# Kernel tuning notes

Hardware: AMD Instinct MI355X
Metric: run time of the kernel (lower is better)

Reference implementation:

```python
import jax, jax.numpy as jnp
import numpy as np

B, S, D, H, PF = 2, 2048, 1024, 16, 4096
HD = D // H
EPS = 1e-5


def _rope_tables(seq_len, dim, theta=10000.0):
    freqs = 1.0 / (theta ** (np.arange(0, dim, 2)[: dim // 2].astype(np.float32) / dim))
    ang = np.outer(np.arange(seq_len, dtype=np.float32), freqs)  # [S, D/2]
    return jnp.asarray(np.cos(ang)), jnp.asarray(np.sin(ang))


def setup_inputs() -> dict:
    key = jax.random.key(0)
    ks = jax.random.split(key, 16)
    s = 0.02
    inp = {
        "src": jax.random.normal(ks[0], (B, S, D), dtype=jnp.float32),
        "Wq": jax.random.normal(ks[1], (D, D), dtype=jnp.float32) * s,
        "bq": jnp.zeros((D,), jnp.float32),
        "Wk": jax.random.normal(ks[2], (D, D), dtype=jnp.float32) * s,
        "bk": jnp.zeros((D,), jnp.float32),
        "Wv": jax.random.normal(ks[3], (D, D), dtype=jnp.float32) * s,
        "bv": jnp.zeros((D,), jnp.float32),
        "Wo": jax.random.normal(ks[4], (D, D), dtype=jnp.float32) * s,
        "bo": jnp.zeros((D,), jnp.float32),
        "ln1_g": jnp.ones((D,), jnp.float32),
        "ln1_b": jnp.zeros((D,), jnp.float32),
        "W1": jax.random.normal(ks[5], (D, PF), dtype=jnp.float32) * s,
        "b1": jnp.zeros((PF,), jnp.float32),
        "W2": jax.random.normal(ks[6], (PF, D), dtype=jnp.float32) * s,
        "b2": jnp.zeros((D,), jnp.float32),
        "ln2_g": jnp.ones((D,), jnp.float32),
        "ln2_b": jnp.zeros((D,), jnp.float32),
    }
    cos, sin = _rope_tables(S, D)
    inp["rope_cos"] = cos
    inp["rope_sin"] = sin
    return inp


def _apply_rope(x, cos, sin):
    # x: [B, S, D]; rotate adjacent channel pairs as complex numbers (Meta LLaMA style)
    xp = x.reshape(x.shape[0], x.shape[1], -1, 2)
    a, b = xp[..., 0], xp[..., 1]
    c = cos[None, : x.shape[1]]
    s = sin[None, : x.shape[1]]
    out = jnp.stack([a * c - b * s, a * s + b * c], axis=-1)
    return out.reshape(x.shape)


def _layer_norm(x, g, b):
    mu = x.mean(-1, keepdims=True)
    var = ((x - mu) ** 2).mean(-1, keepdims=True)
    return (x - mu) * jax.lax.rsqrt(var + EPS) * g + b


def reference(src, Wq, bq, Wk, bk, Wv, bv, Wo, bo, ln1_g, ln1_b,
              W1, b1, W2, b2, ln2_g, ln2_b, rope_cos, rope_sin):
    bsz, seq, _ = src.shape
    Q = src @ Wq + bq
    K = src @ Wk + bk
    V = src @ Wv + bv
    Q = _apply_rope(Q, rope_cos, rope_sin)
    K = _apply_rope(K, rope_cos, rope_sin)
    # split heads: [B, H, S, HD]
    Q = Q.reshape(bsz, seq, H, HD).transpose(0, 2, 1, 3)
    K = K.reshape(bsz, seq, H, HD).transpose(0, 2, 1, 3)
    V = V.reshape(bsz, seq, H, HD).transpose(0, 2, 1, 3)
    scale = 1.0 / jnp.sqrt(jnp.float32(HD))
    energy = jnp.einsum("bhqd,bhkd->bhqk", Q, K) * scale
    attn = jax.nn.softmax(energy, axis=-1)
    x = jnp.einsum("bhqk,bhkd->bhqd", attn, V)
    x = x.transpose(0, 2, 1, 3).reshape(bsz, seq, D)
    attn_out = x @ Wo + bo
    # residual + LayerNorm
    h = _layer_norm(src + attn_out, ln1_g, ln1_b)
    # positionwise feedforward
    ff = jax.nn.relu(h @ W1 + b1) @ W2 + b2
    return _layer_norm(h + ff, ln2_g, ln2_b)
```

## Files before the change

kernel.cpp:

```cpp
#include <hip/hip_runtime.h>

#define SEQ 2048
#define DIM 1024
#define NH 16
#define HDIM 64
#define PFF 4096
#define NROWS 4096
#define BATCH 2
#define NQKV 3072

typedef unsigned short u16;
typedef unsigned int u32;
typedef __attribute__((ext_vector_type(8))) short short8;
typedef __attribute__((ext_vector_type(4))) float f32x4;
typedef __attribute__((ext_vector_type(16))) float f32x16;

__device__ inline float b2f(u16 u){ return __uint_as_float(((u32)u)<<16); }
__device__ inline u16 f2b(float f){
  u32 u = __float_as_uint(f);
  u32 r = u + 0x7FFFu + ((u>>16)&1u);
  return (u16)(r>>16);
}
__device__ __forceinline__ float fexp2(float x){
  float r; asm("v_exp_f32 %0, %1" : "=v"(r) : "v"(x)); return r;
}

#define AS1C(p) ((const __attribute__((address_space(1))) unsigned int*)(p))
#define AS3P(p) ((__attribute__((address_space(3))) unsigned int*)(p))

__global__ __launch_bounds__(256) void k_prep(
    const float* __restrict__ src, u16* __restrict__ Xbf,
    const float* __restrict__ Wq, const float* __restrict__ Wk,
    const float* __restrict__ Wv, const float* __restrict__ Wo,
    u16* __restrict__ WqkvT, u16* __restrict__ WoT,
    const float* __restrict__ W1, u16* __restrict__ W1T,
    const float* __restrict__ W2, u16* __restrict__ W2T,
    const float* __restrict__ bq, const float* __restrict__ bk,
    const float* __restrict__ bv, float* __restrict__ bqkv){
  __shared__ float tile[32][33];
  const int lid = blockIdx.x, tid = threadIdx.x;
  if (lid < 4096){
    int i = lid*256 + tid;
    float4 v = ((const float4*)src)[i];
    ushort4 o;
    o.x = f2b(v.x); o.y = f2b(v.y); o.z = f2b(v.z); o.w = f2b(v.w);
    ((ushort4*)Xbf)[i] = o;
    return;
  }
  int tx = tid & 31, ty = tid >> 5;
  if (lid < 8192){
    int rem = lid - 4096;
    int z = rem >> 10; rem &= 1023;
    const float* in = z==0 ? Wq : (z==1 ? Wk : (z==2 ? Wv : Wo));
    u16* out = (z<3) ? (WqkvT + (size_t)z*DIM*DIM) : WoT;
    int c0 = (rem & 31)*32, r0 = (rem >> 5)*32;
    #pragma unroll
    for (int i=0;i<4;++i)
      tile[ty+i*8][tx] = in[(size_t)(r0+ty+i*8)*DIM + c0 + tx];
    __syncthreads();
    #pragma unroll
    for (int i=0;i<4;++i)
      out[(size_t)(c0+ty+i*8)*DIM + r0 + tx] = f2b(tile[tx][ty+i*8]);
    return;
  }
  if (lid < 12288){
    int rem = lid - 8192;
    int c0 = (rem & 127)*32, r0 = (rem >> 7)*32;
    #pragma unroll
    for (int i=0;i<4;++i)
      tile[ty+i*8][tx] = W1[(size_t)(r0+ty+i*8)*PFF + c0 + tx];
    __syncthreads();
    #pragma unroll
    for (int i=0;i<4;++i)
      W1T[(size_t)(c0+ty+i*8)*DIM + r0 + tx] = f2b(tile[tx][ty+i*8]);
    return;
  }
  if (lid < 16384){
    int rem = lid - 12288;
    int c0 = (rem & 31)*32, r0 = (rem >> 5)*32;
    #pragma unroll
    for (int i=0;i<4;++i)
      tile[ty+i*8][tx] = W2[(size_t)(r0+ty+i*8)*DIM + c0 + tx];
    __syncthreads();
    #pragma unroll
    for (int i=0;i<4;++i)
      W2T[(size_t)(c0+ty+i*8)*PFF + r0 + tx] = f2b(tile[tx][ty+i*8]);
    return;
  }
  {
    int i = (lid - 16384)*256 + tid;
    if (i < NQKV)
      bqkv[i] = i < 1024 ? bq[i] : (i < 2048 ? bk[i-1024] : bv[i-2048]);
  }
}

template<bool RELU, bool BF16OUT, int SPLIT>
__global__ __launch_bounds__(512, 2) void k_gemm256(
    const u16* __restrict__ A, const u16* __restrict__ Bt,
    const float* __restrict__ bias, void* __restrict__ Cp,
    int M, int N, int Kc, int lda, int ldb){
  extern __shared__ char lds[];
  const int tid = threadIdx.x;
  const int lane = tid & 63, wid = tid >> 6;
  const int quad = lane >> 4, l15 = lane & 15;
  const int wm = wid >> 2, wn = wid & 3;
  const int ro = (l15*4 + quad)*16;
  const int srow = lane >> 2;
  const int sk   = (lane & 3)*8;
  const int nwg = gridDim.x * gridDim.y;
  int lid = blockIdx.y * gridDim.x + blockIdx.x;
  lid = (lid & 7) * (nwg >> 3) + (lid >> 3);
  const int bx = lid % gridDim.x, by = lid / gridDim.x;
  const int rowBase = by*256, colBase = bx*256;
  const u16* Az = A  + (size_t)blockIdx.z * Kc;
  const u16* Bz = Bt + (size_t)blockIdx.z * Kc;

  f32x4 acc[8][4] = {};

  auto stage2 = [&](int buf, int k0, int i){
    int idx = i*8 + wid;
    int rs = idx >> 1, ks = idx & 1;
    const u16* ga = Az + (size_t)(rowBase + rs*16 + srow)*lda + k0 + ks*32 + sk;
    __builtin_amdgcn_global_load_lds(AS1C(ga), AS3P(lds + buf*65536 + idx*1024), 16, 0, 0);
    const u16* gb = Bz + (size_t)(colBase + rs*16 + srow)*ldb + k0 + ks*32 + sk;
    __builtin_amdgcn_global_load_lds(AS1C(gb), AS3P(lds + buf*65536 + 32768 + idx*1024), 16, 0, 0);
  };

  #pragma unroll
  for (int i=0;i<4;++i) stage2(0, 0, i);
  __syncthreads();

  const int NT = Kc >> 6;
  #pragma unroll 1
  for (int t=0; t<NT; ++t){
    const int buf = t & 1;
    const bool pf = (t+1 < NT);
    const int k0n = (t+1)*64;
    char* Ab = lds + buf*65536;
    char* Bb = Ab + 32768;
    short8 a0[4][2], a1[4][2], b0[2][2], b1[2][2];

    #pragma unroll
    for (int mf=0; mf<4; ++mf)
      #pragma unroll
      for (int kk=0; kk<2; ++kk)
        a0[mf][kk] = *(const short8*)(Ab + ((wm*8+mf)*2+kk)*1024 + ro);
    #pragma unroll
    for (int nf=0; nf<2; ++nf)
      #pragma unroll
      for (int kk=0; kk<2; ++kk)
        b0[nf][kk] = *(const short8*)(Bb + ((wn*4+nf)*2+kk)*1024 + ro);
    if (pf){ stage2(buf^1, k0n, 0); stage2(buf^1, k0n, 1); }
    __builtin_amdgcn_s_barrier();
    __builtin_amdgcn_s_setprio(1);
    #pragma unroll
    for (int mf=0; mf<4; ++mf)
      #pragma unroll
      for (int nf=0; nf<2; ++nf)
        #pragma unroll
        for (int kk=0; kk<2; ++kk)
          acc[mf][nf] = __builtin_amdgcn_mfma_f32_16x16x32_bf16(a0[mf][kk], b0[nf][kk], acc[mf][nf], 0,0,0);
    __builtin_amdgcn_s_setprio(0);
    __builtin_amdgcn_s_barrier();

    #pragma unroll
    for (int nf=0; nf<2; ++nf)
      #pragma unroll
      for (int kk=0; kk<2; ++kk)
        b1[nf][kk] = *(const short8*)(Bb + ((wn*4+2+nf)*2+kk)*1024 + ro);
    if (pf){ stage2(buf^1, k0n, 2); stage2(buf^1, k0n, 3); }
    __builtin_amdgcn_s_barrier();
    __builtin_amdgcn_s_setprio(1);
    #pragma unroll
    for (int mf=0; mf<4; ++mf)
      #pragma unroll
      for (int nf=0; nf<2; ++nf)
        #pragma unroll
        for (int kk=0; kk<2; ++kk)
          acc[mf][2+nf] = __builtin_amdgcn_mfma_f32_16x16x32_bf16(a0[mf][kk], b1[nf][kk], acc[mf][2+nf], 0,0,0);
    __builtin_amdgcn_s_setprio(0);
    __builtin_amdgcn_s_barrier();

    #pragma unroll
    for (int mf=0; mf<4; ++mf)
      #pragma unroll
      for (int kk=0; kk<2; ++kk)
        a1[mf][kk] = *(const short8*)(Ab + ((wm*8+4+mf)*2+kk)*1024 + ro);
    __builtin_amdgcn_s_barrier();
    __builtin_amdgcn_s_setprio(1);
    #pragma unroll
    for (int mf=0; mf<4; ++mf)
      #pragma unroll
      for (int nf=0; nf<2; ++nf)
        #pragma unroll
        for (int kk=0; kk<2; ++kk)
          acc[4+mf][2+nf] = __builtin_amdgcn_mfma_f32_16x16x32_bf16(a1[mf][kk], b1[nf][kk], acc[4+mf][2+nf], 0,0,0);
    __builtin_amdgcn_s_setprio(0);
    __builtin_amdgcn_s_barrier();

    __builtin_amdgcn_s_setprio(1);
    #pragma unroll
    for (int mf=0; mf<4; ++mf)
      #pragma unroll
      for (int nf=0; nf<2; ++nf)
        #pragma unroll
        for (int kk=0; kk<2; ++kk)
          acc[4+mf][nf] = __builtin_amdgcn_mfma_f32_16x16x32_bf16(a1[mf][kk], b0[nf][kk], acc[4+mf][nf], 0,0,0);
    __builtin_amdgcn_s_setprio(0);
    if (pf) asm volatile("s_waitcnt vmcnt(0)" ::: "memory");
    __builtin_amdgcn_s_barrier();
  }

  u16* Cb = (u16*)Cp + (SPLIT > 1 ? (size_t)blockIdx.z * M * N : 0);
  float* Cf = (float*)Cp + (SPLIT > 1 ? (size_t)blockIdx.z * M * N : 0);
  #pragma unroll
  for (int mf=0; mf<8; ++mf){
    #pragma unroll
    for (int nf=0; nf<4; ++nf){
      int col = colBase + wn*64 + nf*16 + l15;
      float bv = (SPLIT == 1 || blockIdx.z == 0) ? bias[col] : 0.f;
      #pragma unroll
      for (int j=0; j<4; ++j){
        int row = rowBase + wm*128 + mf*16 + quad*4 + j;
        float v = acc[mf][nf][j] + bv;
        if (RELU) v = fmaxf(v, 0.f);
        if (BF16OUT) Cb[(size_t)row*N + col] = f2b(v);
        else         Cf[(size_t)row*N + col] = v;
      }
    }
  }
}

__global__ __launch_bounds__(256) void k_rope_tv(
    u16* __restrict__ QKV, u16* __restrict__ VT,
    const float* __restrict__ cosT, const float* __restrict__ sinT){
  __shared__ u16 tile[32][34];
  const int lid = blockIdx.x, tid = threadIdx.x;
  if (lid < 8192){
    int idx = lid*256 + tid;
    int row = idx >> 9, p = idx & 511;
    int s = row & (SEQ-1);
    float c = cosT[s*512 + p], sn = sinT[s*512 + p];
    u16* qp = QKV + (size_t)row*NQKV + 2*p;
    u16* kp = qp + 1024;
    ushort2 q = *(ushort2*)qp;
    ushort2 k = *(ushort2*)kp;
    float qx = b2f(q.x), qy = b2f(q.y), kx = b2f(k.x), ky = b2f(k.y);
    const float scale = 0.125f * 1.44269504f;
    ushort2 qo, ko;
    qo.x = f2b((qx*c - qy*sn)*scale);
    qo.y = f2b((qx*sn + qy*c)*scale);
    ko.x = f2b(kx*c - ky*sn);
    ko.y = f2b(kx*sn + ky*c);
    *(ushort2*)qp = qo;
    *(ushort2*)kp = ko;
    return;
  }
  int rem = lid - 8192;
  int tx = tid & 31, ty = tid >> 5;
  int d0 = (rem & 31)*32, r0 = (rem >> 5)*32;
  #pragma unroll
  for (int i=0;i<4;++i)
    tile[ty+i*8][tx] = QKV[(size_t)(r0+ty+i*8)*NQKV + 2048 + d0 + tx];
  __syncthreads();
  #pragma unroll
  for (int i=0;i<4;++i)
    VT[(size_t)(d0+ty+i*8)*NROWS + r0 + tx] = tile[tx][ty+i*8];
}

__global__ __launch_bounds__(512) void k_attn(
    const u16* __restrict__ QKV, const u16* __restrict__ VT, u16* __restrict__ Xo){
  const int p = blockIdx.x;
  const int qt = (p >> 3) & 7;
  const int g  = (p & 7) + 8*(p >> 6);
  const int h  = g & 15, b = g >> 4;
  const int tid = threadIdx.x, lane = tid & 63, wid = tid >> 6;
  const int l31 = lane & 31, hi = lane >> 5;
  __shared__ __align__(16) char lds[32768];
  const int srow = lane >> 3, scol = lane & 7;

  short8 qf[4];
  {
    const u16* qrow = QKV + (size_t)(b*SEQ + qt*256 + wid*32 + l31)*NQKV + h*HDIM;
    #pragma unroll
    for (int dk=0; dk<4; ++dk)
      qf[dk] = *(const short8*)(qrow + dk*16 + 8*hi);
  }
  float s_run = 0.f;
  f32x16 oacc[2] = {};
  const size_t krow0 = (size_t)(b*SEQ);

  auto do_stage = [&](int buf, int kt){
    char* kdst = lds + buf*16384;
    char* vdst = kdst + 8192;
    int row = wid*8 + srow;
    int c = scol ^ (row & 7);
    const u16* gk = QKV + (krow0 + kt*64 + row)*NQKV + 1024 + h*HDIM + c*8;
    __builtin_amdgcn_global_load_lds(AS1C(gk), AS3P(kdst + wid*1024), 16, 0, 0);
    const u16* gv = VT + (size_t)(h*HDIM + row)*NROWS + b*SEQ + kt*64 + c*8;
    __builtin_amdgcn_global_load_lds(AS1C(gv), AS3P(vdst + wid*1024), 16, 0, 0);
  };

  auto do_tile = [&](int buf){
    char* kb = lds + buf*16384;
    char* vb = kb + 8192;
    f32x16 pacc[2] = {};
    __builtin_amdgcn_s_setprio(1);
    #pragma unroll
    for (int kbk=0;kbk<2;++kbk){
      #pragma unroll
      for (int dk=0;dk<4;++dk){
        int row = kbk*32 + l31;
        short8 kf = *(const short8*)(kb + ((row*128 + dk*32 + 16*hi) ^ ((row&7)<<4)));
        pacc[kbk] = __builtin_amdgcn_mfma_f32_32x32x16_bf16(kf, qf[dk], pacc[kbk], 0,0,0);
      }
    }
    __builtin_amdgcn_s_setprio(0);
    float psum = 0.f;
    short8 pa[4];
    #pragma unroll
    for (int kbk=0;kbk<2;++kbk){
      #pragma unroll
      for (int s=0;s<2;++s){
        float e0 = fexp2(pacc[kbk][8*s+0]);
        float e1 = fexp2(pacc[kbk][8*s+1]);
        float e2 = fexp2(pacc[kbk][8*s+2]);
        float e3 = fexp2(pacc[kbk][8*s+3]);
        float e4 = fexp2(pacc[kbk][8*s+4]);
        float e5 = fexp2(pacc[kbk][8*s+5]);
        float e6 = fexp2(pacc[kbk][8*s+6]);
        float e7 = fexp2(pacc[kbk][8*s+7]);
        psum += (e0+e1)+(e2+e3)+((e4+e5)+(e6+e7));
        u32 X0, X1, Y0, Y1;
        asm("v_cvt_pk_bf16_f32 %0, %1, %2" : "=v"(X0) : "v"(e0), "v"(e1));
        asm("v_cvt_pk_bf16_f32 %0, %1, %2" : "=v"(X1) : "v"(e2), "v"(e3));
        asm("v_cvt_pk_bf16_f32 %0, %1, %2" : "=v"(Y0) : "v"(e4), "v"(e5));
        asm("v_cvt_pk_bf16_f32 %0, %1, %2" : "=v"(Y1) : "v"(e6), "v"(e7));
        asm volatile("v_permlane32_swap_b32 %0, %1" : "+v"(X0), "+v"(Y0));
        asm volatile("v_permlane32_swap_b32 %0, %1" : "+v"(X1), "+v"(Y1));
        union { u32 w[4]; short8 s8; } pu;
        pu.w[0] = X0; pu.w[1] = X1; pu.w[2] = Y0; pu.w[3] = Y1;
        pa[2*kbk+s] = pu.s8;
      }
    }
    s_run += psum;
    __builtin_amdgcn_s_setprio(1);
    #pragma unroll
    for (int db=0;db<2;++db){
      #pragma unroll
      for (int ks=0;ks<4;++ks){
        int row = db*32 + l31;
        short8 vf = *(const short8*)(vb + ((row*128 + ks*32 + 16*hi) ^ ((row&7)<<4)));
        oacc[db] = __builtin_amdgcn_mfma_f32_32x32x16_bf16(pa[ks], vf, oacc[db], 0,0,0);
      }
    }
    __builtin_amdgcn_s_setprio(0);
  };

  do_stage(0, 0);
  __syncthreads();
  const int NT = SEQ/64;
  #pragma unroll 1
  for (int kt=0; kt<NT; kt+=2){
    do_stage(1, kt+1);
    do_tile(0);
    __syncthreads();
    if (kt+2 < NT) do_stage(0, kt+2);
    do_tile(1);
    __syncthreads();
  }
  s_run += __shfl_xor(s_run, 32);
  #pragma unroll
  for (int r=0;r<16;++r){
    int crow = (r&3) + 8*(r>>2) + 4*hi;
    float sq = __shfl(s_run, crow);
    float rs = __builtin_amdgcn_rcpf(sq);
    int grow = b*SEQ + qt*256 + wid*32 + crow;
    Xo[(size_t)grow*DIM + h*HDIM + l31]      = f2b(oacc[0][r] * rs);
    Xo[(size_t)grow*DIM + h*HDIM + 32 + l31] = f2b(oacc[1][r] * rs);
  }
}

template<int PARTS, bool WF32, bool WBF, bool RESBF>
__global__ __launch_bounds__(256) void k_lnp(
    const void* __restrict__ a, const u16* __restrict__ p,
    const float* __restrict__ g, const float* __restrict__ be,
    float* __restrict__ outf, u16* __restrict__ outb){
  const int row = blockIdx.x, tid = threadIdx.x;
  __shared__ float red[8];
  float x0, x1, x2, x3;
  if (RESBF){
    ushort4 av = ((const ushort4*)((const u16*)a + (size_t)row*DIM))[tid];
    x0 = b2f(av.x); x1 = b2f(av.y); x2 = b2f(av.z); x3 = b2f(av.w);
  } else {
    float4 av = ((const float4*)((const float*)a + (size_t)row*DIM))[tid];
    x0 = av.x; x1 = av.y; x2 = av.z; x3 = av.w;
  }
  #pragma unroll
  for (int z=0; z<PARTS; ++z){
    ushort4 pv = ((const ushort4*)(p + (size_t)z*NROWS*DIM + (size_t)row*DIM))[tid];
    x0 += b2f(pv.x); x1 += b2f(pv.y); x2 += b2f(pv.z); x3 += b2f(pv.w);
  }
  float s = x0+x1+x2+x3;
  #pragma unroll
  for (int o=32;o>=1;o>>=1) s += __shfl_down(s, o);
  if ((tid&63)==0) red[tid>>6] = s;
  __syncthreads();
  float mean = (red[0]+red[1]+red[2]+red[3]) * (1.0f/DIM);
  float d0=x0-mean, d1=x1-mean, d2=x2-mean, d3=x3-mean;
  float vs = d0*d0+d1*d1+d2*d2+d3*d3;
  #pragma unroll
  for (int o=32;o>=1;o>>=1) vs += __shfl_down(vs, o);
  if ((tid&63)==0) red[4+(tid>>6)] = vs;
  __syncthreads();
  float var = (red[4]+red[5]+red[6]+red[7]) * (1.0f/DIM);
  float rs = rsqrtf(var + 1e-5f);
  float4 gv = ((const float4*)g)[tid];
  float4 bev = ((const float4*)be)[tid];
  float4 y;
  y.x = d0*rs*gv.x + bev.x;
  y.y = d1*rs*gv.y + bev.y;
  y.z = d2*rs*gv.z + bev.z;
  y.w = d3*rs*gv.w + bev.w;
  if (WF32)
    ((float4*)(outf + (size_t)row*DIM))[tid] = y;
  if (WBF){
    ushort4 o4; o4.x=f2b(y.x); o4.y=f2b(y.y); o4.z=f2b(y.z); o4.w=f2b(y.w);
    ((ushort4*)(outb + (size_t)row*DIM))[tid] = o4;
  }
}

extern "C" void kernel_launch(void* const* d_in, const int* in_sizes, int n_in,
                              void* d_out, int out_size, void* d_ws, size_t ws_size,
                              hipStream_t stream){
  (void)in_sizes; (void)n_in; (void)out_size; (void)ws_size;
  const float* src  = (const float*)d_in[0];
  const float* Wq   = (const float*)d_in[1];
  const float* bq   = (const float*)d_in[2];
  const float* Wk   = (const float*)d_in[3];
  const float* bk   = (const float*)d_in[4];
  const float* Wv   = (const float*)d_in[5];
  const float* bv   = (const float*)d_in[6];
  const float* Wo   = (const float*)d_in[7];
  const float* bo   = (const float*)d_in[8];
  const float* ln1g = (const float*)d_in[9];
  const float* ln1b = (const float*)d_in[10];
  const float* W1   = (const float*)d_in[11];
  const float* b1   = (const float*)d_in[12];
  const float* W2   = (const float*)d_in[13];
  const float* b2   = (const float*)d_in[14];
  const float* ln2g = (const float*)d_in[15];
  const float* ln2b = (const float*)d_in[16];
  const float* rc   = (const float*)d_in[17];
  const float* rsn  = (const float*)d_in[18];

  char* ws = (char*)d_ws;
  const size_t MB = (size_t)1<<20;
  u16* Xbf   = (u16*)(ws);
  u16* QKV   = (u16*)(ws + 8*MB);
  u16* VTb   = (u16*)(ws + 32*MB);
  u16* aob   = (u16*)(ws + 8*MB);
  u16* ff2b  = (u16*)(ws + 8*MB);
  u16* xat   = (u16*)(ws + 40*MB);
  u16* hbf   = (u16*)(ws + 48*MB);
  u16* WqkvT = (u16*)(ws + 56*MB);
  u16* WoT   = (u16*)(ws + 62*MB);
  u16* W1T   = (u16*)(ws + 64*MB);
  u16* W2T   = (u16*)(ws + 72*MB);
  u16* ff1   = (u16*)(ws + 80*MB);
  float* bqkv= (float*)(ws + 128*MB);

  hipFuncSetAttribute((const void*)&k_gemm256<false,true,1>,
                      hipFuncAttributeMaxDynamicSharedMemorySize, 131072);
  hipFuncSetAttribute((const void*)&k_gemm256<true,true,1>,
                      hipFuncAttributeMaxDynamicSharedMemorySize, 131072);
  hipFuncSetAttribute((const void*)&k_gemm256<false,true,4>,
                      hipFuncAttributeMaxDynamicSharedMemorySize, 131072);

  dim3 blk(256);
  k_prep<<<dim3(16396), blk, 0, stream>>>(src, Xbf, Wq, Wk, Wv, Wo, WqkvT, WoT,
                                          W1, W1T, W2, W2T, bq, bk, bv, bqkv);
  k_gemm256<false,true,1><<<dim3(NQKV/256, NROWS/256), dim3(512), 131072, stream>>>(
      Xbf, WqkvT, bqkv, QKV, NROWS, NQKV, DIM, DIM, DIM);
  k_rope_tv<<<dim3(12288), blk, 0, stream>>>(QKV, VTb, rc, rsn);
  k_attn<<<dim3(256), dim3(512), 0, stream>>>(QKV, VTb, xat);
  k_gemm256<false,true,4><<<dim3(DIM/256, NROWS/256, 4), dim3(512), 131072, stream>>>(
      xat, WoT, bo, aob, NROWS, DIM, 256, DIM, DIM);
  k_lnp<4,false,true,false><<<dim3(NROWS), blk, 0, stream>>>(
      src, aob, ln1g, ln1b, nullptr, hbf);
  k_gemm256<true,true,1><<<dim3(PFF/256, NROWS/256), dim3(512), 131072, stream>>>(
      hbf, W1T, b1, ff1, NROWS, PFF, DIM, DIM, DIM);
  k_gemm256<false,true,4><<<dim3(DIM/256, NROWS/256, 4), dim3(512), 131072, stream>>>(
      ff1, W2T, b2, ff2b, NROWS, DIM, 1024, PFF, PFF);
  k_lnp<4,true,false,true><<<dim3(NROWS), blk, 0, stream>>>(
      hbf, ff2b, ln2g, ln2b, (float*)d_out, nullptr);
}
```

Measured before the change: 229.3 us.

## Halve GEMM K-tile to 32 to shrink LDS and raise occupancy

```diff
diff --git a/kernel.cpp b/kernel.cpp
--- a/kernel.cpp
+++ b/kernel.cpp
@@ -95,7 +95,7 @@
 }
 
 template<bool RELU, bool BF16OUT, int SPLIT>
-__global__ __launch_bounds__(512, 2) void k_gemm256(
+__global__ __launch_bounds__(512, 4) void k_gemm256(
     const u16* __restrict__ A, const u16* __restrict__ Bt,
     const float* __restrict__ bias, void* __restrict__ Cp,
     int M, int N, int Kc, int lda, int ldb){
@@ -119,93 +119,54 @@
 
   auto stage2 = [&](int buf, int k0, int i){
     int idx = i*8 + wid;
-    int rs = idx >> 1, ks = idx & 1;
-    const u16* ga = Az + (size_t)(rowBase + rs*16 + srow)*lda + k0 + ks*32 + sk;
-    __builtin_amdgcn_global_load_lds(AS1C(ga), AS3P(lds + buf*65536 + idx*1024), 16, 0, 0);
-    const u16* gb = Bz + (size_t)(colBase + rs*16 + srow)*ldb + k0 + ks*32 + sk;
-    __builtin_amdgcn_global_load_lds(AS1C(gb), AS3P(lds + buf*65536 + 32768 + idx*1024), 16, 0, 0);
+    const u16* ga = Az + (size_t)(rowBase + idx*16 + srow)*lda + k0 + sk;
+    __builtin_amdgcn_global_load_lds(AS1C(ga), AS3P(lds + buf*32768 + idx*1024), 16, 0, 0);
+    const u16* gb = Bz + (size_t)(colBase + idx*16 + srow)*ldb + k0 + sk;
+    __builtin_amdgcn_global_load_lds(AS1C(gb), AS3P(lds + buf*32768 + 16384 + idx*1024), 16, 0, 0);
   };
 
-  #pragma unroll
-  for (int i=0;i<4;++i) stage2(0, 0, i);
+  stage2(0, 0, 0);
+  stage2(0, 0, 1);
   __syncthreads();
 
-  const int NT = Kc >> 6;
+  const int NT = Kc >> 5;
   #pragma unroll 1
   for (int t=0; t<NT; ++t){
     const int buf = t & 1;
     const bool pf = (t+1 < NT);
-    const int k0n = (t+1)*64;
-    char* Ab = lds + buf*65536;
-    char* Bb = Ab + 32768;
-    short8 a0[4][2], a1[4][2], b0[2][2], b1[2][2];
+    const int k0n = (t+1)*32;
+    char* Ab = lds + buf*32768;
+    char* Bb = Ab + 16384;
+    short8 a0[4], a1[4], bb[4];
 
     #pragma unroll
     for (int mf=0; mf<4; ++mf)
-      #pragma unroll
-      for (int kk=0; kk<2; ++kk)
-        a0[mf][kk] = *(const short8*)(Ab + ((wm*8+mf)*2+kk)*1024 + ro);
-    #pragma unroll
-    for (int nf=0; nf<2; ++nf)
-      #pragma unroll
-      for (int kk=0; kk<2; ++kk)
-        b0[nf][kk] = *(const short8*)(Bb + ((wn*4+nf)*2+kk)*1024 + ro);
-    if (pf){ stage2(buf^1, k0n, 0); stage2(buf^1, k0n, 1); }
+      a0[mf] = *(const short8*)(Ab + (wm*8+mf)*1024 + ro);
+    #pragma unroll
+    for (int nf=0; nf<4; ++nf)
+      bb[nf] = *(const short8*)(Bb + (wn*4+nf)*1024 + ro);
+    if (pf) stage2(buf^1, k0n, 0);
     __builtin_amdgcn_s_barrier();
     __builtin_amdgcn_s_setprio(1);
     #pragma unroll
     for (int mf=0; mf<4; ++mf)
       #pragma unroll
-      for (int nf=0; nf<2; ++nf)
-        #pragma unroll
-        for (int kk=0; kk<2; ++kk)
-          acc[mf][nf] = __builtin_amdgcn_mfma_f32_16x16x32_bf16(a0[mf][kk], b0[nf][kk], acc[mf][nf], 0,0,0);
+      for (int nf=0; nf<4; ++nf)
+        acc[mf][nf] = __builtin_amdgcn_mfma_f32_16x16x32_bf16(a0[mf], bb[nf], acc[mf][nf], 0,0,0);
     __builtin_amdgcn_s_setprio(0);
     __builtin_amdgcn_s_barrier();
 
     #pragma unroll
-    for (int nf=0; nf<2; ++nf)
-      #pragma unroll
-      for (int kk=0; kk<2; ++kk)
-        b1[nf][kk] = *(const short8*)(Bb + ((wn*4+2+nf)*2+kk)*1024 + ro);
-    if (pf){ stage2(buf^1, k0n, 2); stage2(buf^1, k0n, 3); }
+    for (int mf=0; mf<4; ++mf)
+      a1[mf] = *(const short8*)(Ab + (wm*8+4+mf)*1024 + ro);
+    if (pf) stage2(buf^1, k0n, 1);
     __builtin_amdgcn_s_barrier();
     __builtin_amdgcn_s_setprio(1);
     #pragma unroll
     for (int mf=0; mf<4; ++mf)
       #pragma unroll
-      for (int nf=0; nf<2; ++nf)
-        #pragma unroll
-        for (int kk=0; kk<2; ++kk)
-          acc[mf][2+nf] = __builtin_amdgcn_mfma_f32_16x16x32_bf16(a0[mf][kk], b1[nf][kk], acc[mf][2+nf], 0,0,0);
-    __builtin_amdgcn_s_setprio(0);
-    __builtin_amdgcn_s_barrier();
-
-    #pragma unroll
-    for (int mf=0; mf<4; ++mf)
-      #pragma unroll
-      for (int kk=0; kk<2; ++kk)
-        a1[mf][kk] = *(const short8*)(Ab + ((wm*8+4+mf)*2+kk)*1024 + ro);
-    __builtin_amdgcn_s_barrier();
-    __builtin_amdgcn_s_setprio(1);
-    #pragma unroll
-    for (int mf=0; mf<4; ++mf)
-      #pragma unroll
-      for (int nf=0; nf<2; ++nf)
-        #pragma unroll
-        for (int kk=0; kk<2; ++kk)
-          acc[4+mf][2+nf] = __builtin_amdgcn_mfma_f32_16x16x32_bf16(a1[mf][kk], b1[nf][kk], acc[4+mf][2+nf], 0,0,0);
-    __builtin_amdgcn_s_setprio(0);
-    __builtin_amdgcn_s_barrier();
-
-    __builtin_amdgcn_s_setprio(1);
-    #pragma unroll
-    for (int mf=0; mf<4; ++mf)
-      #pragma unroll
-      for (int nf=0; nf<2; ++nf)
-        #pragma unroll
-        for (int kk=0; kk<2; ++kk)
-          acc[4+mf][nf] = __builtin_amdgcn_mfma_f32_16x16x32_bf16(a1[mf][kk], b0[nf][kk], acc[4+mf][nf], 0,0,0);
+      for (int nf=0; nf<4; ++nf)
+        acc[4+mf][nf] = __builtin_amdgcn_mfma_f32_16x16x32_bf16(a1[mf], bb[nf], acc[4+mf][nf], 0,0,0);
     __builtin_amdgcn_s_setprio(0);
     if (pf) asm volatile("s_waitcnt vmcnt(0)" ::: "memory");
     __builtin_amdgcn_s_barrier();
@@ -471,26 +432,26 @@
   float* bqkv= (float*)(ws + 128*MB);
 
   hipFuncSetAttribute((const void*)&k_gemm256<false,true,1>,
-                      hipFuncAttributeMaxDynamicSharedMemorySize, 131072);
+                      hipFuncAttributeMaxDynamicSharedMemorySize, 65536);
   hipFuncSetAttribute((const void*)&k_gemm256<true,true,1>,
-                      hipFuncAttributeMaxDynamicSharedMemorySize, 131072);
+                      hipFuncAttributeMaxDynamicSharedMemorySize, 65536);
   hipFuncSetAttribute((const void*)&k_gemm256<false,true,4>,
-                      hipFuncAttributeMaxDynamicSharedMemorySize, 131072);
+                      hipFuncAttributeMaxDynamicSharedMemorySize, 65536);
 
   dim3 blk(256);
   k_prep<<<dim3(16396), blk, 0, stream>>>(src, Xbf, Wq, Wk, Wv, Wo, WqkvT, WoT,
                                           W1, W1T, W2, W2T, bq, bk, bv, bqkv);
-  k_gemm256<false,true,1><<<dim3(NQKV/256, NROWS/256), dim3(512), 131072, stream>>>(
+  k_gemm256<false,true,1><<<dim3(NQKV/256, NROWS/256), dim3(512), 65536, stream>>>(
       Xbf, WqkvT, bqkv, QKV, NROWS, NQKV, DIM, DIM, DIM);
   k_rope_tv<<<dim3(12288), blk, 0, stream>>>(QKV, VTb, rc, rsn);
   k_attn<<<dim3(256), dim3(512), 0, stream>>>(QKV, VTb, xat);
-  k_gemm256<false,true,4><<<dim3(DIM/256, NROWS/256, 4), dim3(512), 131072, stream>>>(
+  k_gemm256<false,true,4><<<dim3(DIM/256, NROWS/256, 4), dim3(512), 65536, stream>>>(
       xat, WoT, bo, aob, NROWS, DIM, 256, DIM, DIM);
   k_lnp<4,false,true,false><<<dim3(NROWS), blk, 0, stream>>>(
       src, aob, ln1g, ln1b, nullptr, hbf);
-  k_gemm256<true,true,1><<<dim3(PFF/256, NROWS/256), dim3(512), 131072, stream>>>(
+  k_gemm256<true,true,1><<<dim3(PFF/256, NROWS/256), dim3(512), 65536, stream>>>(
       hbf, W1T, b1, ff1, NROWS, PFF, DIM, DIM, DIM);
-  k_gemm256<false,true,4><<<dim3(DIM/256, NROWS/256, 4), dim3(512), 131072, stream>>>(
+  k_gemm256<false,true,4><<<dim3(DIM/256, NROWS/256, 4), dim3(512), 65536, stream>>>(
       ff1, W2T, b2, ff2b, NROWS, DIM, 1024, PFF, PFF);
   k_lnp<4,true,false,true><<<dim3(NROWS), blk, 0, stream>>>(
       hbf, ff2b, ln2g, ln2b, (float*)d_out, nullptr);
```

New measurement: 910.3 us. 297% more time.
